# Performance work log

Hardware: AMD Instinct MI355X
Metric: run time of the kernel (lower is better)

## Reference

```python
import jax, jax.numpy as jnp
from jax import lax
import numpy as np

# hyperparams (from init_kwargs)
NB_CLASSES = 100
SZ_EMBED = 128
SCALE = 3.0
LAM = 0.7          # np.random.beta(1,1) draw, fixed for determinism
OT_EPS = 0.05
SINK_THRESH = 0.1
SINK_MAX_ITER = 100
DN = ('NCHW', 'OIHW', 'NCHW')


def l2norm(x, axis):
    # F.normalize: x / max(||x||, 1e-12)
    n = jnp.sqrt(jnp.sum(x * x, axis=axis, keepdims=True))
    return x / jnp.maximum(n, 1e-12)


def encode(x, W_enc, W_feat):
    c = jax.nn.relu(lax.conv_general_dilated(x, W_enc, (2, 2), 'SAME', dimension_numbers=DN))
    f = jax.nn.relu(lax.conv_general_dilated(c, W_feat, (1, 1), 'SAME', dimension_numbers=DN))
    feat = f.mean(axis=(2, 3))  # (B, SZ_EMBED)
    return c, feat


def decode(c, W_dec):
    return lax.conv_transpose(c, W_dec, (2, 2), 'SAME', dimension_numbers=DN)


def sinkhorn(K, u, v):
    # faithful to torch loop: update r, c; break when mean|r-r0| < thresh
    def cond(s):
        i, r, c, err = s
        return jnp.logical_and(i < SINK_MAX_ITER, err >= SINK_THRESH)

    def body(s):
        i, r, c, _ = s
        r0 = r
        r = u / jnp.einsum('bij,bj->bi', K, c)
        c = v / jnp.einsum('bji,bj->bi', K, r)
        err = jnp.mean(jnp.abs(r - r0))
        return (i + 1, r, c, err)

    init = (jnp.int32(0), jnp.ones_like(u), jnp.ones_like(v), jnp.array(jnp.inf, K.dtype))
    _, r, c, _ = lax.while_loop(cond, body, init)
    return r[:, :, None] * c[:, None, :] * K  # (B, S, S)


def pair_wise_wdist(x, y):
    B, C, H, W = x.shape
    S = H * W
    xf = l2norm(x.reshape(B, C, S), axis=1)  # unit vectors per spatial location
    yf = l2norm(y.reshape(B, C, S), axis=1)
    sim = jnp.einsum('bcs,bcm->bsm', xf, yf)  # (B, S, S)
    # ||x-y||^2 = 2 - 2*sim for unit vectors (avoids (B,C,S,S) intermediate)
    dist1 = jnp.sqrt(jnp.maximum(2.0 - 2.0 * sim, 0.0) + 1e-6)
    u = jnp.full((B, S), 1.0 / S, dtype=sim.dtype)
    v = jnp.full((B, S), 1.0 / S, dtype=sim.dtype)
    K = lax.stop_gradient(jnp.exp(-(1.0 - sim) / OT_EPS))  # torch.no_grad
    T = lax.stop_gradient(sinkhorn(K, u, v))
    dist = jnp.sum(T * dist1, axis=(1, 2))
    return dist, T


def metric_loss(X, labels, P):
    Pn = SCALE * l2norm(P, axis=-1)
    Xn = SCALE * l2norm(X, axis=-1)
    # squared pairwise distance X vs P
    D = (jnp.sum(Xn * Xn, -1)[:, None] + jnp.sum(Pn * Pn, -1)[None, :]
         - 2.0 * Xn @ Pn.T)
    logp = jax.nn.log_softmax(-D, axis=-1)
    # smoothing_const=0 -> one-hot labels
    return -jnp.mean(logp[jnp.arange(X.shape[0]), labels])


def reference(xa, xb, la, lb, proxies, W_enc, W_feat, W_dec):
    B, C, H, W = xa.shape
    c_xa, feat_xa = encode(xa, W_enc, W_feat)
    xa_hat = decode(c_xa, W_dec)
    c_xb, feat_xb = encode(xb, W_enc, W_feat)
    xb_hat = decode(c_xb, W_dec)

    struct_dist, T = pair_wise_wdist(xa, xb)

    xa_fl = l2norm(xa, axis=1).reshape(B, C, -1)
    xb_fl = l2norm(xb, axis=1).reshape(B, C, -1)
    # faithful to the original einsum (k and j summed independently)
    xb_tomix = jnp.einsum('bmk,bji->bmi', xa_fl, T)
    xa_tomix = jnp.einsum('bmk,bji->bmi', xb_fl, jnp.swapaxes(T, 1, 2))

    lam = LAM
    mixed_xa = (lam * xa.reshape(B, C, -1) + (1 - lam) * xa_tomix).reshape(B, C, H, W)
    mixed_xb = (lam * xb.reshape(B, C, -1) + (1 - lam) * xb_tomix).reshape(B, C, H, W)

    l_x_rec_a = jnp.mean(jnp.square(xa_hat - xa))
    l_x_rec_b = jnp.mean(jnp.square(xb_hat - xb))

    feat_ma = mixed_xa.mean(axis=(2, 3))  # adaptive_avg_pool2d -> (B, C)
    feat_mb = mixed_xb.mean(axis=(2, 3))

    l_c_rec_a = metric_loss(feat_xa, la, proxies)
    l_c_rec_b = metric_loss(feat_xb, lb, proxies)
    l_c_rec_ma = lam * metric_loss(feat_ma, la, proxies) + (1 - lam) * metric_loss(feat_ma, lb, proxies)
    l_c_rec_mb = lam * metric_loss(feat_mb, lb, proxies) + (1 - lam) * metric_loss(feat_mb, la, proxies)

    l_total = l_x_rec_a + l_x_rec_b + l_c_rec_a + l_c_rec_b + l_c_rec_ma + l_c_rec_mb
    return jnp.stack([l_total, l_x_rec_a, l_x_rec_b, l_c_rec_a, l_c_rec_b, l_c_rec_ma, l_c_rec_mb])


def setup_inputs() -> dict:
    key = jax.random.key(0)
    ks = jax.random.split(key, 8)
    B, C, H, W = 32, 128, 32, 32
    xa = jax.random.normal(ks[0], (B, C, H, W), jnp.float32)
    xb = jax.random.normal(ks[1], (B, C, H, W), jnp.float32)
    la = jax.random.randint(ks[2], (B,), 0, NB_CLASSES)
    lb = jax.random.randint(ks[3], (B,), 0, NB_CLASSES)
    proxies = jax.random.normal(ks[4], (NB_CLASSES, SZ_EMBED), jnp.float32) / 8.0
    W_enc = jax.random.normal(ks[5], (2 * C, C, 3, 3), jnp.float32) * 0.02
    W_feat = jax.random.normal(ks[6], (SZ_EMBED, 2 * C, 3, 3), jnp.float32) * 0.02
    W_dec = jax.random.normal(ks[7], (C, 2 * C, 3, 3), jnp.float32) * 0.02
    return {"xa": xa, "xb": xb, "la": la, "lb": lb, "proxies": proxies,
            "W_enc": W_enc, "W_feat": W_feat, "W_dec": W_dec}
```

## Files before the change

kernel.cpp:

```cpp
#include <hip/hip_runtime.h>
#include <hip/hip_bf16.h>

#define DEVI __device__ __forceinline__

constexpr int B_ = 32, CI = 128, CM = 256, H_ = 32, W_ = 32;
constexpr int S_ = 1024, NB = 100;
constexpr float LAMF = 0.7f, ILAMF = 0.3f, SCALEF = 3.0f;
constexpr size_t XSZ = (size_t)32 * 16 * 1156 * 8;
constexpr size_t XBS = (size_t)16 * 1156 * 8;
constexpr size_t CSZ = (size_t)32 * 32 * 324 * 8;
constexpr size_t CBS = (size_t)32 * 324 * 8;

typedef short bf8 __attribute__((ext_vector_type(8)));
typedef float f4 __attribute__((ext_vector_type(4)));
typedef float f16v __attribute__((ext_vector_type(16)));
typedef unsigned short u16;
typedef unsigned int u32;

struct alignas(8) us4 { u16 v[4]; };
struct alignas(16) us8 { u16 v[8]; };

__device__ __constant__ int TAPD9c[9] = {0, 2, 6, 8, 1, 7, 3, 5, 4};

DEVI u16 f2bf(float f) {
    unsigned u = __builtin_bit_cast(unsigned, f);
    u += 0x7FFFu + ((u >> 16) & 1u);
    return (u16)(u >> 16);
}
DEVI float bf2f(u16 h) {
    unsigned u = ((unsigned)h) << 16;
    return __builtin_bit_cast(float, u);
}

DEVI void gll16(const void* g, void* l) {
    __builtin_amdgcn_global_load_lds(
        (const __attribute__((address_space(1))) u32*)g,
        (__attribute__((address_space(3))) u32*)l, 16, 0, 0);
}

DEVI float waveSum(float v) {
#pragma unroll
    for (int off = 32; off > 0; off >>= 1) v += __shfl_down(v, off, 64);
    return v;
}
DEVI float blockSum256(float v, float* lds4) {
    v = waveSum(v);
    int wid = threadIdx.x >> 6, lane = threadIdx.x & 63;
    __syncthreads();
    if (lane == 0) lds4[wid] = v;
    __syncthreads();
    return lds4[0] + lds4[1] + lds4[2] + lds4[3];
}
DEVI float blockSum128(float v, float* lds2) {
    v = waveSum(v);
    int wid = threadIdx.x >> 6, lane = threadIdx.x & 63;
    __syncthreads();
    if (lane == 0) lds2[wid] = v;
    __syncthreads();
    return lds2[0] + lds2[1];
}
DEVI float blockMax128(float v, float* lds2) {
#pragma unroll
    for (int off = 32; off > 0; off >>= 1) v = fmaxf(v, __shfl_down(v, off, 64));
    int wid = threadIdx.x >> 6, lane = threadIdx.x & 63;
    __syncthreads();
    if (lane == 0) lds2[wid] = v;
    __syncthreads();
    return fmaxf(lds2[0], lds2[1]);
}

__global__ __launch_bounds__(256) void k_prep_w(const float* __restrict__ We,
                                                const float* __restrict__ Wf,
                                                const float* __restrict__ Wd,
                                                u16* __restrict__ A1p,
                                                u16* __restrict__ A2p,
                                                u16* __restrict__ A3p) {
    int i = blockIdx.x * 256 + threadIdx.x;
    {
        int e = i & 7, s = (i >> 3) & 511, j = i >> 12;
        int Mt = j / 36, kc = j - Mt * 36;
        int tap = kc >> 2, cq = kc & 3;
        int q = s >> 7, m = s & 127;
        int oc = Mt * 128 + m, ch = cq * 32 + q * 8 + e;
        A1p[i] = f2bf(We[((size_t)oc * CI + ch) * 9 + tap]);
    }
    {
        int e = i & 7, s = (i >> 3) & 511, kc = i >> 12;
        int tapi = kc >> 3, cq = kc & 7;
        int q = s >> 7, m = s & 127;
        int ch = cq * 32 + q * 8 + e;
        A2p[i] = f2bf(Wf[((size_t)m * CM + ch) * 9 + tapi]);
        A3p[i] = f2bf(Wd[((size_t)m * CM + ch) * 9 + TAPD9c[tapi]]);
    }
}

__global__ __launch_bounds__(128) void k_prox(const float* __restrict__ P,
                                              float* __restrict__ PnT,
                                              float* __restrict__ pn2) {
    __shared__ float lds2[2];
    int k = blockIdx.x, t = threadIdx.x;
    float v = P[k * CI + t];
    float ss = blockSum128(v * v, lds2);
    float sc = SCALEF / fmaxf(sqrtf(ss), 1e-12f);
    float pv = v * sc;
    PnT[t * NB + k] = pv;
    float s2 = blockSum128(pv * pv, lds2);
    if (t == 0) pn2[k] = s2;
}

__global__ __launch_bounds__(256) void k_ring(u16* __restrict__ xpad, u16* __restrict__ cpad) {
    int b = blockIdx.x, ab = blockIdx.y, t = threadIdx.x;
    u16* xp = xpad + (size_t)ab * XSZ + (size_t)b * XBS;
    u16* cp = cpad + (size_t)ab * CSZ + (size_t)b * CBS;
    us8 z = {};
    for (int i = t; i < 132 * 16; i += 256) {
        int cc = i / 132, rp = i - cc * 132;
        int pos;
        if (rp < 68) pos = (rp < 34) ? (32 * 34 + rp) : (33 * 34 + rp - 34);
        else { int r2 = rp - 68; pos = (r2 >> 1) * 34 + 32 + (r2 & 1); }
        *(us8*)(xp + ((size_t)cc * 1156 + pos) * 8) = z;
    }
    for (int i = t; i < 68 * 32; i += 256) {
        int cc = i / 68, rp = i - cc * 68;
        int pos;
        if (rp < 36) pos = (rp < 18) ? rp : (17 * 18 + rp - 18);
        else { int r2 = rp - 36; pos = (1 + (r2 >> 1)) * 18 + ((r2 & 1) ? 17 : 0); }
        *(us8*)(cp + ((size_t)cc * 324 + pos) * 8) = z;
    }
}

__global__ __launch_bounds__(256) void k_xpose(const float* __restrict__ xa,
                                               const float* __restrict__ xb,
                                               u16* __restrict__ xpad,
                                               float* __restrict__ mpart) {
    __shared__ float ldsx[128][64];
    __shared__ float sred[256];
    __shared__ float sinv[64];
    int b = blockIdx.x, yg = blockIdx.y, ab = blockIdx.z;
    int t = threadIdx.x;
    const float* x = (ab ? xb : xa) + (size_t)b * CI * S_ + yg * 64;
    int c4 = t >> 6, p = t & 63;
    for (int c0 = 0; c0 < 32; ++c0) {
        int c = c0 * 4 + c4;
        ldsx[c][p] = x[(size_t)c * S_ + p];
    }
    __syncthreads();
    int qc = t >> 6;
    int y = yg * 2 + (p >> 5), xcol = p & 31;
    u16* ox = xpad + (size_t)ab * XSZ + (size_t)b * XBS;
    float ss = 0.f;
#pragma unroll
    for (int c8 = 0; c8 < 4; ++c8) {
        int cb = qc * 32 + c8 * 8;
        int cc = cb >> 3;
        us8 pk;
#pragma unroll
        for (int j = 0; j < 8; ++j) {
            float v = ldsx[cb + j][p];
            ss = fmaf(v, v, ss);
            pk.v[j] = f2bf(v);
        }
        *(us8*)(ox + ((size_t)cc * 1156 + y * 34 + xcol) * 8) = pk;
    }
    sred[t] = ss;
    __syncthreads();
    if (t < 64) {
        float s = sred[t] + sred[t + 64] + sred[t + 128] + sred[t + 192];
        sinv[t] = 1.f / fmaxf(sqrtf(s), 1e-12f);
    }
    __syncthreads();
    int c = t >> 1, h = t & 1;
    float sx = 0.f, sf = 0.f;
    for (int i = 0; i < 32; ++i) {
        int p2 = h * 32 + ((i + c) & 31);
        float v = ldsx[c][p2];
        sx += v;
        sf = fmaf(v, sinv[p2], sf);
    }
    sx += __shfl_xor(sx, 1, 64);
    sf += __shfl_xor(sf, 1, 64);
    if (!(t & 1)) {
        size_t base = ((size_t)(ab * 32 + b) * 16 + yg) * 128 + c;
        mpart[base] = sx * (1.f / 1024.f);
        mpart[(size_t)2 * 32 * 16 * 128 * 2 / 2 + base] = sf * (1.f / 1024.f);
    }
}

__global__ __launch_bounds__(256, 2) void k_conv1g(const u16* __restrict__ XC,
                                                   const u16* __restrict__ A1p,
                                                   u16* __restrict__ CC) {
    __shared__ u16 sA[2][8192];
    __shared__ u16 sB[2][4096];
    int t = threadIdx.x, l = t & 63, l15 = l & 15, lq = l >> 4, w = t >> 6;
    int wm = w & 1, wn = w >> 1;
    int Nt = blockIdx.x, b = blockIdx.y;
    int ab = blockIdx.z & 1, Mt = blockIdx.z >> 1;
    const u16* xc = XC + (size_t)ab * XSZ + (size_t)b * XBS;
    const u16* Ag = A1p + (size_t)Mt * (36 * 4096);
    int bpos0 = (8 * Nt + 2 * (l >> 4)) * 34 + 2 * (l & 15);
    const int po1[9] = {0, 1, 2, 34, 35, 36, 68, 69, 70};

    auto stageA = [&](int buf, int kcA) {
        const u16* ga = Ag + (size_t)kcA * 4096 + t * 8;
        u16* da = &sA[buf][w * 512];
#pragma unroll
        for (int i = 0; i < 4; ++i) gll16(ga + i * 2048, da + i * 2048);
    };
    auto stageB = [&](int buf, int po, int s) {
#pragma unroll
        for (int i = 0; i < 2; ++i) {
            int ks = i * 4 + w;
            gll16(xc + ((size_t)(s * 8 + ks) * 1156 + bpos0 + po) * 8,
                  &sB[buf][(size_t)ks * 512]);
        }
    };

    f4 acc[4][2] = {};
    stageA(0, 0);
    stageB(0, 0, 0);
    int cur = 0;
#pragma unroll
    for (int ti = 0; ti < 9; ++ti) {
        const int po = po1[ti];
        const int poN = (ti < 8) ? po1[ti + 1] : 0;
#pragma unroll 1
        for (int s = 0; s < 2; ++s) {
            __syncthreads();
            bool last = (ti == 8) && (s == 1);
            if (!last) {
                int tin = (s < 1) ? ti : ti + 1;
                int sn = (s < 1) ? 1 : 0;
                stageA(cur ^ 1, tin * 4 + sn * 2);
                stageB(cur ^ 1, (s < 1) ? po : poN, sn);
            }
            const u16* As = sA[cur];
            const u16* Bs = sB[cur];
#pragma unroll
            for (int kc2 = 0; kc2 < 2; ++kc2) {
                bf8 af[4], bv[2];
#pragma unroll
                for (int mf = 0; mf < 4; ++mf)
                    af[mf] = *(const bf8*)(As + ((kc2 * 4 + lq) * 128 + wm * 64 + mf * 16 + l15) * 8);
#pragma unroll
                for (int nf = 0; nf < 2; ++nf)
                    bv[nf] = *(const bf8*)(Bs + ((kc2 * 4 + lq) * 64 + wn * 32 + nf * 16 + l15) * 8);
#pragma unroll
                for (int mf = 0; mf < 4; ++mf)
#pragma unroll
                    for (int nf = 0; nf < 2; ++nf)
                        acc[mf][nf] = __builtin_amdgcn_mfma_f32_16x16x32_bf16(af[mf], bv[nf], acc[mf][nf], 0, 0, 0);
            }
            cur ^= 1;
        }
    }
    u16* cb = CC + (size_t)ab * CSZ + (size_t)b * CBS;
#pragma unroll
    for (int mf = 0; mf < 4; ++mf) {
        int mc = Mt * 128 + wm * 64 + mf * 16 + lq * 4;
#pragma unroll
        for (int nf = 0; nf < 2; ++nf) {
            int nl = wn * 32 + nf * 16 + l15;
            int oh = Nt * 4 + (nl >> 4), ow = nl & 15;
            int posO = (1 + oh) * 18 + 1 + ow;
            us4 pk;
#pragma unroll
            for (int r = 0; r < 4; ++r) pk.v[r] = f2bf(fmaxf(acc[mf][nf][r], 0.f));
            *(us4*)(cb + ((size_t)(mc >> 3) * 324 + posO) * 8 + (mc & 7)) = pk;
        }
    }
}


#define KSTEP(ACC, KYV, KXV, HN, KCAN)                                              \
    {                                                                               \
        __syncthreads();                                                            \
        if (HN) stageA(cur ^ 1, (KCAN));                                            \
        const u16* As = sA[cur];                                                    \
        _Pragma("unroll") for (int kc2 = 0; kc2 < 2; ++kc2) {                       \
            _Pragma("unroll") for (int j = 0; j < 2; ++j) {                         \
                bf8 a0 = *(const bf8*)(As + kc2 * 4096 + j * 2048 + aBase);         \
                bf8 a1 = *(const bf8*)(As + kc2 * 4096 + j * 2048 + aBase + 256);   \
                const u16* bp = sS + (kc2 * 720 + j * 360) * 8 + bBase;             \
                bf8 b0 = *(const bf8*)(bp + (((KYV)) * 18 + (KXV)) * 8);            \
                bf8 b1 = *(const bf8*)(bp + (((KYV) + 2) * 18 + (KXV)) * 8);        \
                ACC[0][0] = __builtin_amdgcn_mfma_f32_32x32x16_bf16(a0, b0, ACC[0][0], 0, 0, 0); \
                ACC[0][1] = __builtin_amdgcn_mfma_f32_32x32x16_bf16(a0, b1, ACC[0][1], 0, 0, 0); \
                ACC[1][0] = __builtin_amdgcn_mfma_f32_32x32x16_bf16(a1, b0, ACC[1][0], 0, 0, 0); \
                ACC[1][1] = __builtin_amdgcn_mfma_f32_32x32x16_bf16(a1, b1, ACC[1][1], 0, 0, 0); \
            }                                                                       \
        }                                                                           \
        cur ^= 1;                                                                   \
    }

#define FLUSH(ACC, PY, PX)                                                          \
    _Pragma("unroll") for (int mf = 0; mf < 2; ++mf) {                              \
        _Pragma("unroll") for (int nf = 0; nf < 2; ++nf) {                          \
            int n = wn * 64 + nf * 32 + l31;                                        \
            int oh = 8 * Nt + (n >> 4), ow = n & 15;                                \
            int Y = 2 * oh + (PY), X = 2 * ow + (PX);                               \
            _Pragma("unroll") for (int rg = 0; rg < 4; ++rg) {                      \
                int mc = wm * 64 + mf * 32 + 8 * rg + 4 * lh;                       \
                us4 xv = *(const us4*)(xq + (size_t)(mc >> 3) * 1156 * 8 +          \
                                       (size_t)(Y * 34 + X) * 8 + (mc & 7));        \
                _Pragma("unroll") for (int r = 0; r < 4; ++r) {                     \
                    float d = ACC[mf][nf][rg * 4 + r] - bf2f(xv.v[r]);              \
                    ss = fmaf(d, d, ss);                                            \
                }                                                                   \
            }                                                                       \
        }                                                                           \
    }

__global__ __launch_bounds__(256, 2) void k_cde11(const u16* __restrict__ CC,
                                                  const u16* __restrict__ A2p,
                                                  const u16* __restrict__ A3p,
                                                  const u16* __restrict__ XC,
                                                  float* __restrict__ pc0,
                                                  float* __restrict__ pc1,
                                                  float* __restrict__ prpart) {
    __shared__ u16 sS[11520];
    __shared__ u16 sA[2][8192];
    __shared__ float lds4[4];
    int t = threadIdx.x, l = t & 63, l31 = l & 31, lh = l >> 5, w = t >> 6;
    int wm = w & 1, wn = w >> 1;
    int Nt = blockIdx.x, b = blockIdx.y;
    int ab = blockIdx.z & 1, unit = blockIdx.z >> 1;
    const u16* cbb = CC + (size_t)ab * CSZ + (size_t)b * CBS;
    const u16* xq = XC + (size_t)ab * XSZ + (size_t)b * XBS;
    const u16* Ag = (unit < 2) ? A2p : A3p;
    int r0 = 8 * Nt;
    int aBase = (lh * 128 + wm * 64 + l31) * 8;
    int bBase = (lh * 180 + (wn * 4 + (l31 >> 4)) * 18 + (l31 & 15)) * 8;

    auto stageA = [&](int buf, int kcA) {
        const u16* ga = Ag + (size_t)kcA * 4096 + t * 8;
        u16* da = &sA[buf][w * 512];
#pragma unroll
        for (int i = 0; i < 4; ++i) gll16(ga + i * 2048, da + i * 2048);
    };
    auto stage_slab = [&](int seg) {
        if (t < 180) {
            int cc0 = (seg >> 1) * 16 + (seg & 1) * 8;
#pragma unroll 1
            for (int ccL = 0; ccL < 8; ++ccL) {
                us8 v = *(const us8*)(cbb + ((size_t)(cc0 + ccL) * 324 + r0 * 18 + t) * 8);
                *(us8*)(sS + ((size_t)ccL * 180 + t) * 8) = v;
            }
        }
    };

    int cur = 0;
    float ss = 0.f;
    if (unit < 2) {
        f16v acc[2][2] = {};
        int segBase = unit * 2;
        stage_slab(segBase);
        stageA(0, (segBase >> 1) * 4 + (segBase & 1) * 2);
#pragma unroll
        for (int sl = 0; sl < 2; ++sl) {
            int seg = segBase + sl;
            if (sl) { __syncthreads(); stage_slab(seg); }
#pragma unroll 1
            for (int tap = 0; tap < 9; ++tap) {
                int s = sl * 9 + tap;
                int ky = tap / 3, kx = tap - ky * 3;
                bool hn = s < 17;
                int s1 = hn ? s + 1 : 0;
                int sl1 = s1 / 9, tap1 = s1 - sl1 * 9;
                int seg1 = segBase + sl1;
                int kcan = tap1 * 8 + (seg1 >> 1) * 4 + (seg1 & 1) * 2;
                KSTEP(acc, ky, kx, hn, kcan);
            }
        }
        float* pw = (unit == 0 ? pc0 : pc1) + (size_t)(ab * 32 + b) * 128 * 256;
#pragma unroll
        for (int mf = 0; mf < 2; ++mf)
#pragma unroll
            for (int nf = 0; nf < 2; ++nf)
#pragma unroll
                for (int reg = 0; reg < 16; ++reg) {
                    int oc = wm * 64 + mf * 32 + (reg & 3) + 8 * (reg >> 2) + 4 * lh;
                    int pos = 128 * Nt + wn * 64 + nf * 32 + l31;
                    pw[(size_t)oc * 256 + pos] = acc[mf][nf][reg];
                }
    } else if (unit == 2) {
        f16v accP[2][2] = {}, accQ[2][2] = {};
        stage_slab(0);
        stageA(0, 0);
#pragma unroll
        for (int seg = 0; seg < 4; ++seg) {
            if (seg) { __syncthreads(); stage_slab(seg); }
#pragma unroll 1
            for (int r = 0; r < 5; ++r) {
                int s = seg * 5 + r;
                bool hn = s < 19;
                int s1 = hn ? s + 1 : 0;
                int seg1 = s1 / 5, r1 = s1 - seg1 * 5;
                int tapi1 = (r1 < 4) ? r1 : 8;
                int kcan = tapi1 * 8 + (seg1 >> 1) * 4 + (seg1 & 1) * 2;
                if (r < 4) {
                    int dy = r >> 1, dx = r & 1;
                    KSTEP(accP, dy, dx, hn, kcan);
                } else {
                    KSTEP(accQ, 1, 1, hn, kcan);
                }
            }
        }
        FLUSH(accP, 0, 0);
        FLUSH(accQ, 1, 1);
        ss = blockSum256(ss, lds4);
        if (t == 0) prpart[ab * 128 + Nt * 32 + b] = ss;
    } else {
        f16v accP[2][2] = {}, accQ[2][2] = {};
        stage_slab(0);
        stageA(0, 32);
#pragma unroll
        for (int seg = 0; seg < 4; ++seg) {
            if (seg) { __syncthreads(); stage_slab(seg); }
#pragma unroll 1
            for (int r = 0; r < 4; ++r) {
                int s = seg * 4 + r;
                bool hn = s < 15;
                int s1 = hn ? s + 1 : 0;
                int seg1 = s1 >> 2, r1 = s1 & 3;
                int kcan = (4 + r1) * 8 + (seg1 >> 1) * 4 + (seg1 & 1) * 2;
                if (r < 2) {
                    KSTEP(accP, r, 1, hn, kcan);
                } else {
                    KSTEP(accQ, 1, r - 2, hn, kcan);
                }
            }
        }
        FLUSH(accP, 0, 1);
        FLUSH(accQ, 1, 0);
        ss = blockSum256(ss, lds4);
        if (t == 0) prpart[ab * 128 + 64 + Nt * 32 + b] = ss;
    }
}

#undef KSTEP
#undef FLUSH

__global__ __launch_bounds__(256) void k_cfin(const float* __restrict__ pc0,
                                              const float* __restrict__ pc1,
                                              float* __restrict__ feats) {
    __shared__ float lds4[4];
    int ocg = blockIdx.x, b = blockIdx.y, ab = blockIdx.z;
    int t = threadIdx.x;
    const float* p0 = pc0 + (size_t)(ab * 32 + b) * 128 * 256;
    const float* p1 = pc1 + (size_t)(ab * 32 + b) * 128 * 256;
    float* fo = feats + (size_t)(ab * 32 + b) * 128;
#pragma unroll 1
    for (int i = 0; i < 16; ++i) {
        int oc = ocg * 16 + i;
        float v = fmaxf(p0[(size_t)oc * 256 + t] + p1[(size_t)oc * 256 + t], 0.f);
        float s = blockSum256(v, lds4);
        if (t == 0) fo[oc] = s * (1.f / 256.f);
    }
}

constexpr size_t MPK = (size_t)2 * 32 * 16 * 128;

__global__ __launch_bounds__(128) void k_metric(const float* __restrict__ feats,
                                                const float* __restrict__ mpart,
                                                const float* __restrict__ PnT,
                                                const float* __restrict__ pn2,
                                                const int* __restrict__ la,
                                                const int* __restrict__ lb,
                                                float* __restrict__ mo) {
    __shared__ float lds2[2];
    __shared__ float xs[128];
    int blk = blockIdx.x;
    int t = threadIdx.x;
    int b = blk & 31;
    float xv;
    if (blk < 64) {
        xv = feats[(size_t)blk * CI + t];
    } else {
        int abx = (blk < 96) ? 0 : 1;
        int abf = 1 - abx;
        const float* mx = mpart + ((size_t)(abx * 32 + b) * 16) * 128 + t;
        const float* mf = mpart + MPK + ((size_t)(abf * 32 + b) * 16) * 128 + t;
        float s = 0.f;
#pragma unroll
        for (int yg = 0; yg < 16; ++yg)
            s += LAMF * mx[yg * 128] + ILAMF * mf[yg * 128];
        xv = s;
    }
    float ssq = blockSum128(xv * xv, lds2);
    float sc = SCALEF / fmaxf(sqrtf(ssq), 1e-12f);
    float xn = xv * sc;
    xs[t] = xn;
    float xn2 = blockSum128(xn * xn, lds2);
    bool active = (t < NB);
    float Dk = 1e30f;
    if (active) {
        float dot = 0.f;
#pragma unroll 8
        for (int e = 0; e < CI; ++e) dot = fmaf(xs[e], PnT[e * NB + t], dot);
        Dk = xn2 + pn2[t] - 2.f * dot;
    }
    float z = active ? -Dk : -1e30f;
    float m = blockMax128(z, lds2);
    float e = active ? expf(z - m) : 0.f;
    float se = blockSum128(e, lds2);
    float lse = m + logf(se);
    if (t == 0) mo[blk * 3 + 0] = lse;
    int A = la[b], Bb = lb[b];
    if (t == A) mo[blk * 3 + 1] = Dk;
    if (t == Bb) mo[blk * 3 + 2] = Dk;
}

__global__ __launch_bounds__(128) void k_final(const float* __restrict__ prpart,
                                               const float* __restrict__ mo,
                                               float* __restrict__ out) {
    __shared__ float lds2[2];
    __shared__ float mla[4], mlb[4];
    int t = threadIdx.x;
    float sa = blockSum128(prpart[t], lds2);
    float sb = blockSum128(prpart[128 + t], lds2);
    const float* m = mo + t * 3;
    float ula = m[0] + m[1];
    float ulb = m[0] + m[2];
#pragma unroll
    for (int off = 16; off > 0; off >>= 1) {
        ula += __shfl_down(ula, off, 32);
        ulb += __shfl_down(ulb, off, 32);
    }
    if ((t & 31) == 0) { mla[t >> 5] = ula * (1.f / 32.f); mlb[t >> 5] = ulb * (1.f / 32.f); }
    __syncthreads();
    if (t == 0) {
        float lxa = sa * (1.f / 4194304.f);
        float lxb = sb * (1.f / 4194304.f);
        float lca = mla[0];
        float lcb = mlb[1];
        float lcma = LAMF * mla[2] + ILAMF * mlb[2];
        float lcmb = LAMF * mlb[3] + ILAMF * mla[3];
        out[0] = lxa + lxb + lca + lcb + lcma + lcmb;
        out[1] = lxa; out[2] = lxb; out[3] = lca; out[4] = lcb; out[5] = lcma; out[6] = lcmb;
    }
}

extern "C" void kernel_launch(void* const* d_in, const int* in_sizes, int n_in,
                              void* d_out, int out_size, void* d_ws, size_t ws_size,
                              hipStream_t stream) {
    const float* xa = (const float*)d_in[0];
    const float* xb = (const float*)d_in[1];
    const int* la = (const int*)d_in[2];
    const int* lb = (const int*)d_in[3];
    const float* P = (const float*)d_in[4];
    const float* We = (const float*)d_in[5];
    const float* Wf = (const float*)d_in[6];
    const float* Wd = (const float*)d_in[7];

    char* w = (char*)d_ws;
    const size_t XPAD_B = XSZ * 2 * sizeof(u16);
    const size_t CPAD_B = CSZ * 2 * sizeof(u16);
    const size_t AW_B = (size_t)294912 * 2;
    u16* xpad = (u16*)w;                 w += XPAD_B;
    u16* cpad = (u16*)w;                 w += CPAD_B;
    u16* A1p = (u16*)w;                  w += AW_B;
    u16* A2p = (u16*)w;                  w += AW_B;
    u16* A3p = (u16*)w;                  w += AW_B;
    float* PnT = (float*)w;              w += 12800 * 4;
    float* pn2 = (float*)w;              w += 128 * 4;
    float* feats = (float*)w;            w += 8192 * 4;
    float* mpart = (float*)w;            w += MPK * 2 * 4;
    float* prpart = (float*)w;           w += 256 * 4;
    float* mo = (float*)w;               w += 384 * 4;
    float* pc0 = (float*)w;              w += (size_t)2 * 32 * 128 * 256 * 4;
    float* pc1 = (float*)w;              w += (size_t)2 * 32 * 128 * 256 * 4;
    float* out = (float*)d_out;

    k_prep_w<<<1152, 256, 0, stream>>>(We, Wf, Wd, A1p, A2p, A3p);
    k_prox<<<NB, 128, 0, stream>>>(P, PnT, pn2);
    k_ring<<<dim3(32, 2), 256, 0, stream>>>(xpad, cpad);
    k_xpose<<<dim3(32, 16, 2), 256, 0, stream>>>(xa, xb, xpad, mpart);
    k_conv1g<<<dim3(4, 32, 4), 256, 0, stream>>>(xpad, A1p, cpad);
    k_cde11<<<dim3(2, 32, 8), 256, 0, stream>>>(cpad, A2p, A3p, xpad, pc0, pc1, prpart);
    k_cfin<<<dim3(8, 32, 2), 256, 0, stream>>>(pc0, pc1, feats);
    k_metric<<<128, 128, 0, stream>>>(feats, mpart, PnT, pn2, la, lb, mo);
    k_final<<<1, 128, 0, stream>>>(prpart, mo, out);
}
```

Measured before the change: 99.85 us.

## Merge setup kernels into one launch and fold feature pooling into metric kernel

Four independent setup kernels (weight prep, proxy normalization, zero-ring padding, input transpose) are merged into a single launch, with each branch chosen by block index. The partial-conv outputs are now stored position-major with vector f4 stores. The separate feature-pooling kernel is removed and the ReLU mean over positions is computed inside the metric kernel. This cuts launch count and one global round trip. In exchange, 64 metric blocks each serially read 256x128 values from each of two buffers, which may leave little parallelism for that step.

```diff
diff --git a/kernel.cpp b/kernel.cpp
--- a/kernel.cpp
+++ b/kernel.cpp
@@ -10,6 +10,7 @@
 constexpr size_t XBS = (size_t)16 * 1156 * 8;
 constexpr size_t CSZ = (size_t)32 * 32 * 324 * 8;
 constexpr size_t CBS = (size_t)32 * 324 * 8;
+constexpr size_t MPK = (size_t)2 * 32 * 16 * 128;
 
 typedef short bf8 __attribute__((ext_vector_type(8)));
 typedef float f4 __attribute__((ext_vector_type(4)));
@@ -69,120 +70,130 @@
     return fmaxf(lds2[0], lds2[1]);
 }
 
-__global__ __launch_bounds__(256) void k_prep_w(const float* __restrict__ We,
-                                                const float* __restrict__ Wf,
-                                                const float* __restrict__ Wd,
-                                                u16* __restrict__ A1p,
-                                                u16* __restrict__ A2p,
-                                                u16* __restrict__ A3p) {
-    int i = blockIdx.x * 256 + threadIdx.x;
-    {
-        int e = i & 7, s = (i >> 3) & 511, j = i >> 12;
-        int Mt = j / 36, kc = j - Mt * 36;
-        int tap = kc >> 2, cq = kc & 3;
-        int q = s >> 7, m = s & 127;
-        int oc = Mt * 128 + m, ch = cq * 32 + q * 8 + e;
-        A1p[i] = f2bf(We[((size_t)oc * CI + ch) * 9 + tap]);
-    }
-    {
-        int e = i & 7, s = (i >> 3) & 511, kc = i >> 12;
-        int tapi = kc >> 3, cq = kc & 7;
-        int q = s >> 7, m = s & 127;
-        int ch = cq * 32 + q * 8 + e;
-        A2p[i] = f2bf(Wf[((size_t)m * CM + ch) * 9 + tapi]);
-        A3p[i] = f2bf(Wd[((size_t)m * CM + ch) * 9 + TAPD9c[tapi]]);
-    }
-}
-
-__global__ __launch_bounds__(128) void k_prox(const float* __restrict__ P,
-                                              float* __restrict__ PnT,
-                                              float* __restrict__ pn2) {
-    __shared__ float lds2[2];
-    int k = blockIdx.x, t = threadIdx.x;
-    float v = P[k * CI + t];
-    float ss = blockSum128(v * v, lds2);
-    float sc = SCALEF / fmaxf(sqrtf(ss), 1e-12f);
-    float pv = v * sc;
-    PnT[t * NB + k] = pv;
-    float s2 = blockSum128(pv * pv, lds2);
-    if (t == 0) pn2[k] = s2;
-}
-
-__global__ __launch_bounds__(256) void k_ring(u16* __restrict__ xpad, u16* __restrict__ cpad) {
-    int b = blockIdx.x, ab = blockIdx.y, t = threadIdx.x;
-    u16* xp = xpad + (size_t)ab * XSZ + (size_t)b * XBS;
-    u16* cp = cpad + (size_t)ab * CSZ + (size_t)b * CBS;
-    us8 z = {};
-    for (int i = t; i < 132 * 16; i += 256) {
-        int cc = i / 132, rp = i - cc * 132;
-        int pos;
-        if (rp < 68) pos = (rp < 34) ? (32 * 34 + rp) : (33 * 34 + rp - 34);
-        else { int r2 = rp - 68; pos = (r2 >> 1) * 34 + 32 + (r2 & 1); }
-        *(us8*)(xp + ((size_t)cc * 1156 + pos) * 8) = z;
-    }
-    for (int i = t; i < 68 * 32; i += 256) {
-        int cc = i / 68, rp = i - cc * 68;
-        int pos;
-        if (rp < 36) pos = (rp < 18) ? rp : (17 * 18 + rp - 18);
-        else { int r2 = rp - 36; pos = (1 + (r2 >> 1)) * 18 + ((r2 & 1) ? 17 : 0); }
-        *(us8*)(cp + ((size_t)cc * 324 + pos) * 8) = z;
-    }
-}
-
-__global__ __launch_bounds__(256) void k_xpose(const float* __restrict__ xa,
+__global__ __launch_bounds__(256) void k_setup(const float* __restrict__ xa,
                                                const float* __restrict__ xb,
+                                               const float* __restrict__ P,
+                                               const float* __restrict__ We,
+                                               const float* __restrict__ Wf,
+                                               const float* __restrict__ Wd,
+                                               u16* __restrict__ A1p,
+                                               u16* __restrict__ A2p,
+                                               u16* __restrict__ A3p,
+                                               float* __restrict__ PnT,
+                                               float* __restrict__ pn2,
                                                u16* __restrict__ xpad,
+                                               u16* __restrict__ cpad,
                                                float* __restrict__ mpart) {
     __shared__ float ldsx[128][64];
     __shared__ float sred[256];
     __shared__ float sinv[64];
-    int b = blockIdx.x, yg = blockIdx.y, ab = blockIdx.z;
-    int t = threadIdx.x;
-    const float* x = (ab ? xb : xa) + (size_t)b * CI * S_ + yg * 64;
-    int c4 = t >> 6, p = t & 63;
-    for (int c0 = 0; c0 < 32; ++c0) {
-        int c = c0 * 4 + c4;
-        ldsx[c][p] = x[(size_t)c * S_ + p];
-    }
-    __syncthreads();
-    int qc = t >> 6;
-    int y = yg * 2 + (p >> 5), xcol = p & 31;
-    u16* ox = xpad + (size_t)ab * XSZ + (size_t)b * XBS;
-    float ss = 0.f;
-#pragma unroll
-    for (int c8 = 0; c8 < 4; ++c8) {
-        int cb = qc * 32 + c8 * 8;
-        int cc = cb >> 3;
-        us8 pk;
-#pragma unroll
-        for (int j = 0; j < 8; ++j) {
-            float v = ldsx[cb + j][p];
-            ss = fmaf(v, v, ss);
-            pk.v[j] = f2bf(v);
-        }
-        *(us8*)(ox + ((size_t)cc * 1156 + y * 34 + xcol) * 8) = pk;
-    }
-    sred[t] = ss;
-    __syncthreads();
-    if (t < 64) {
-        float s = sred[t] + sred[t + 64] + sred[t + 128] + sred[t + 192];
-        sinv[t] = 1.f / fmaxf(sqrtf(s), 1e-12f);
-    }
-    __syncthreads();
-    int c = t >> 1, h = t & 1;
-    float sx = 0.f, sf = 0.f;
-    for (int i = 0; i < 32; ++i) {
-        int p2 = h * 32 + ((i + c) & 31);
-        float v = ldsx[c][p2];
-        sx += v;
-        sf = fmaf(v, sinv[p2], sf);
-    }
-    sx += __shfl_xor(sx, 1, 64);
-    sf += __shfl_xor(sf, 1, 64);
-    if (!(t & 1)) {
-        size_t base = ((size_t)(ab * 32 + b) * 16 + yg) * 128 + c;
-        mpart[base] = sx * (1.f / 1024.f);
-        mpart[(size_t)2 * 32 * 16 * 128 * 2 / 2 + base] = sf * (1.f / 1024.f);
+    int bid = blockIdx.x, t = threadIdx.x;
+    if (bid < 1152) {
+        int i = bid * 256 + t;
+        {
+            int e = i & 7, s = (i >> 3) & 511, j = i >> 12;
+            int Mt = j / 36, kc = j - Mt * 36;
+            int tap = kc >> 2, cq = kc & 3;
+            int q = s >> 7, m = s & 127;
+            int oc = Mt * 128 + m, ch = cq * 32 + q * 8 + e;
+            A1p[i] = f2bf(We[((size_t)oc * CI + ch) * 9 + tap]);
+        }
+        {
+            int e = i & 7, s = (i >> 3) & 511, kc = i >> 12;
+            int tapi = kc >> 3, cq = kc & 7;
+            int q = s >> 7, m = s & 127;
+            int ch = cq * 32 + q * 8 + e;
+            A2p[i] = f2bf(Wf[((size_t)m * CM + ch) * 9 + tapi]);
+            A3p[i] = f2bf(Wd[((size_t)m * CM + ch) * 9 + TAPD9c[tapi]]);
+        }
+    } else if (bid < 1202) {
+        int k = 2 * (bid - 1152) + (t >> 7);
+        int lane = t & 127;
+        float v = P[k * CI + lane];
+        float vv = waveSum(v * v);
+        __syncthreads();
+        if ((t & 63) == 0) sred[t >> 6] = vv;
+        __syncthreads();
+        int hb = (t >> 7) * 2;
+        float ss = sred[hb] + sred[hb + 1];
+        float sc = SCALEF / fmaxf(sqrtf(ss), 1e-12f);
+        float pv = v * sc;
+        PnT[lane * NB + k] = pv;
+        float p2 = waveSum(pv * pv);
+        __syncthreads();
+        if ((t & 63) == 0) sred[t >> 6] = p2;
+        __syncthreads();
+        float s2 = sred[hb] + sred[hb + 1];
+        if (lane == 0) pn2[k] = s2;
+    } else if (bid < 1266) {
+        int idx = bid - 1202;
+        int b = idx & 31, ab = idx >> 5;
+        u16* xp = xpad + (size_t)ab * XSZ + (size_t)b * XBS;
+        u16* cp = cpad + (size_t)ab * CSZ + (size_t)b * CBS;
+        us8 z = {};
+        for (int i = t; i < 132 * 16; i += 256) {
+            int cc = i / 132, rp = i - cc * 132;
+            int pos;
+            if (rp < 68) pos = (rp < 34) ? (32 * 34 + rp) : (33 * 34 + rp - 34);
+            else { int r2 = rp - 68; pos = (r2 >> 1) * 34 + 32 + (r2 & 1); }
+            *(us8*)(xp + ((size_t)cc * 1156 + pos) * 8) = z;
+        }
+        for (int i = t; i < 68 * 32; i += 256) {
+            int cc = i / 68, rp = i - cc * 68;
+            int pos;
+            if (rp < 36) pos = (rp < 18) ? rp : (17 * 18 + rp - 18);
+            else { int r2 = rp - 36; pos = (1 + (r2 >> 1)) * 18 + ((r2 & 1) ? 17 : 0); }
+            *(us8*)(cp + ((size_t)cc * 324 + pos) * 8) = z;
+        }
+    } else {
+        int idx = bid - 1266;
+        int b = idx & 31, yg = (idx >> 5) & 15, ab = idx >> 9;
+        const float* x = (ab ? xb : xa) + (size_t)b * CI * S_ + yg * 64;
+        int c4 = t >> 6, p = t & 63;
+        for (int c0 = 0; c0 < 32; ++c0) {
+            int c = c0 * 4 + c4;
+            ldsx[c][p] = x[(size_t)c * S_ + p];
+        }
+        __syncthreads();
+        int qc = t >> 6;
+        int y = yg * 2 + (p >> 5), xcol = p & 31;
+        u16* ox = xpad + (size_t)ab * XSZ + (size_t)b * XBS;
+        float ss = 0.f;
+#pragma unroll
+        for (int c8 = 0; c8 < 4; ++c8) {
+            int cb = qc * 32 + c8 * 8;
+            int cc = cb >> 3;
+            us8 pk;
+#pragma unroll
+            for (int j = 0; j < 8; ++j) {
+                float v = ldsx[cb + j][p];
+                ss = fmaf(v, v, ss);
+                pk.v[j] = f2bf(v);
+            }
+            *(us8*)(ox + ((size_t)cc * 1156 + y * 34 + xcol) * 8) = pk;
+        }
+        sred[t] = ss;
+        __syncthreads();
+        if (t < 64) {
+            float s = sred[t] + sred[t + 64] + sred[t + 128] + sred[t + 192];
+            sinv[t] = 1.f / fmaxf(sqrtf(s), 1e-12f);
+        }
+        __syncthreads();
+        int c = t >> 1, h = t & 1;
+        float sx = 0.f, sf = 0.f;
+        for (int i = 0; i < 32; ++i) {
+            int p2 = h * 32 + ((i + c) & 31);
+            float v = ldsx[c][p2];
+            sx += v;
+            sf = fmaf(v, sinv[p2], sf);
+        }
+        sx += __shfl_xor(sx, 1, 64);
+        sf += __shfl_xor(sf, 1, 64);
+        if (!(t & 1)) {
+            size_t base = ((size_t)(ab * 32 + b) * 16 + yg) * 128 + c;
+            mpart[base] = sx * (1.f / 1024.f);
+            mpart[MPK + base] = sf * (1.f / 1024.f);
+        }
     }
 }
 
@@ -371,17 +382,20 @@
                 KSTEP(acc, ky, kx, hn, kcan);
             }
         }
-        float* pw = (unit == 0 ? pc0 : pc1) + (size_t)(ab * 32 + b) * 128 * 256;
+        float* pw = (unit == 0 ? pc0 : pc1) + (size_t)(ab * 32 + b) * 32768;
 #pragma unroll
         for (int mf = 0; mf < 2; ++mf)
 #pragma unroll
-            for (int nf = 0; nf < 2; ++nf)
-#pragma unroll
-                for (int reg = 0; reg < 16; ++reg) {
-                    int oc = wm * 64 + mf * 32 + (reg & 3) + 8 * (reg >> 2) + 4 * lh;
-                    int pos = 128 * Nt + wn * 64 + nf * 32 + l31;
-                    pw[(size_t)oc * 256 + pos] = acc[mf][nf][reg];
+            for (int nf = 0; nf < 2; ++nf) {
+                int pos = 128 * Nt + wn * 64 + nf * 32 + l31;
+                float* row = pw + (size_t)pos * 128 + wm * 64 + mf * 32 + 4 * lh;
+#pragma unroll
+                for (int g = 0; g < 4; ++g) {
+                    f4 v = {acc[mf][nf][4 * g + 0], acc[mf][nf][4 * g + 1],
+                            acc[mf][nf][4 * g + 2], acc[mf][nf][4 * g + 3]};
+                    *(f4*)(row + 8 * g) = v;
                 }
+            }
     } else if (unit == 2) {
         f16v accP[2][2] = {}, accQ[2][2] = {};
         stage_slab(0);
@@ -440,27 +454,8 @@
 #undef KSTEP
 #undef FLUSH
 
-__global__ __launch_bounds__(256) void k_cfin(const float* __restrict__ pc0,
-                                              const float* __restrict__ pc1,
-                                              float* __restrict__ feats) {
-    __shared__ float lds4[4];
-    int ocg = blockIdx.x, b = blockIdx.y, ab = blockIdx.z;
-    int t = threadIdx.x;
-    const float* p0 = pc0 + (size_t)(ab * 32 + b) * 128 * 256;
-    const float* p1 = pc1 + (size_t)(ab * 32 + b) * 128 * 256;
-    float* fo = feats + (size_t)(ab * 32 + b) * 128;
-#pragma unroll 1
-    for (int i = 0; i < 16; ++i) {
-        int oc = ocg * 16 + i;
-        float v = fmaxf(p0[(size_t)oc * 256 + t] + p1[(size_t)oc * 256 + t], 0.f);
-        float s = blockSum256(v, lds4);
-        if (t == 0) fo[oc] = s * (1.f / 256.f);
-    }
-}
-
-constexpr size_t MPK = (size_t)2 * 32 * 16 * 128;
-
-__global__ __launch_bounds__(128) void k_metric(const float* __restrict__ feats,
+__global__ __launch_bounds__(128) void k_metric(const float* __restrict__ pc0,
+                                                const float* __restrict__ pc1,
                                                 const float* __restrict__ mpart,
                                                 const float* __restrict__ PnT,
                                                 const float* __restrict__ pn2,
@@ -474,7 +469,14 @@
     int b = blk & 31;
     float xv;
     if (blk < 64) {
-        xv = feats[(size_t)blk * CI + t];
+        int ab = blk >> 5;
+        const float* p0 = pc0 + (size_t)(ab * 32 + b) * 32768;
+        const float* p1 = pc1 + (size_t)(ab * 32 + b) * 32768;
+        float s = 0.f;
+#pragma unroll 4
+        for (int pos = 0; pos < 256; ++pos)
+            s += fmaxf(p0[pos * 128 + t] + p1[pos * 128 + t], 0.f);
+        xv = s * (1.f / 256.f);
     } else {
         int abx = (blk < 96) ? 0 : 1;
         int abf = 1 - abx;
@@ -563,7 +565,6 @@
     u16* A3p = (u16*)w;                  w += AW_B;
     float* PnT = (float*)w;              w += 12800 * 4;
     float* pn2 = (float*)w;              w += 128 * 4;
-    float* feats = (float*)w;            w += 8192 * 4;
     float* mpart = (float*)w;            w += MPK * 2 * 4;
     float* prpart = (float*)w;           w += 256 * 4;
     float* mo = (float*)w;               w += 384 * 4;
@@ -571,13 +572,10 @@
     float* pc1 = (float*)w;              w += (size_t)2 * 32 * 128 * 256 * 4;
     float* out = (float*)d_out;
 
-    k_prep_w<<<1152, 256, 0, stream>>>(We, Wf, Wd, A1p, A2p, A3p);
-    k_prox<<<NB, 128, 0, stream>>>(P, PnT, pn2);
-    k_ring<<<dim3(32, 2), 256, 0, stream>>>(xpad, cpad);
-    k_xpose<<<dim3(32, 16, 2), 256, 0, stream>>>(xa, xb, xpad, mpart);
+    k_setup<<<2290, 256, 0, stream>>>(xa, xb, P, We, Wf, Wd, A1p, A2p, A3p,
+                                      PnT, pn2, xpad, cpad, mpart);
     k_conv1g<<<dim3(4, 32, 4), 256, 0, stream>>>(xpad, A1p, cpad);
     k_cde11<<<dim3(2, 32, 8), 256, 0, stream>>>(cpad, A2p, A3p, xpad, pc0, pc1, prpart);
-    k_cfin<<<dim3(8, 32, 2), 256, 0, stream>>>(pc0, pc1, feats);
-    k_metric<<<128, 128, 0, stream>>>(feats, mpart, PnT, pn2, la, lb, mo);
+    k_metric<<<128, 128, 0, stream>>>(pc0, pc1, mpart, PnT, pn2, la, lb, mo);
     k_final<<<1, 128, 0, stream>>>(prpart, mo, out);
 }
```

After: 100.0 us. About the same (+0.2%).
